# Performance work log

Measured on AMD Instinct MI355X. Metric: run time of the kernel, lower is better.

## Reference

```python
import jax, jax.numpy as jnp
import numpy as np

N_NODES = 40000
N_EDGES = 640000
HIDDEN = 128


def setup_inputs() -> dict:
    key = jax.random.key(0)
    k_h, k_w, k_b, k_src, k_dst = jax.random.split(key, 5)
    h = jax.random.normal(k_h, (N_NODES, HIDDEN), dtype=jnp.float32)
    # nn.Linear(hidden_dim, hidden_dim): weight [out, in], bias [out]
    W = jax.random.normal(k_w, (HIDDEN, HIDDEN), dtype=jnp.float32) * (1.0 / np.sqrt(HIDDEN))
    b = jax.random.normal(k_b, (HIDDEN,), dtype=jnp.float32) * 0.01
    src = jax.random.randint(k_src, (N_EDGES,), 0, N_NODES, dtype=jnp.int32)
    dst = jax.random.randint(k_dst, (N_EDGES,), 0, N_NODES, dtype=jnp.int32)
    return {"h": h, "W": W, "b": b, "src": src, "dst": dst}


def reference(h, W, b, src, dst):
    n = h.shape[0]
    # message: gather source node features; reduce: mailbox sum == segment-sum by dst
    agg = jax.ops.segment_sum(h[src], dst, num_segments=n)  # [N, D]
    updated = agg @ W.T + b  # merge_linner
    # DGL update_all only writes nodes with >=1 incoming edge; others keep old h
    indeg = jax.ops.segment_sum(jnp.ones(src.shape, dtype=h.dtype), dst, num_segments=n)
    return jnp.where((indeg > 0)[:, None], updated, h)
```

## Files before the change

### kernel.cpp

```cpp
#include <hip/hip_runtime.h>
#include <hip/hip_bf16.h>

static constexpr int HIDDEN = 128;

using bf16x8 = __attribute__((ext_vector_type(8))) __bf16;
using f32x4 = __attribute__((ext_vector_type(4))) float;
using ushort8v = __attribute__((ext_vector_type(8))) ushort;

__device__ inline ushort f2bf(float x) {
  __hip_bfloat16 t = __float2bfloat16(x);
  return *reinterpret_cast<ushort*>(&t);
}

__global__ void __launch_bounds__(256) hist_wconv_kernel(
    const int* __restrict__ dst, int* __restrict__ counts, int n_edges,
    int nbh, const float* __restrict__ W, ushort* __restrict__ wbf) {
  if (blockIdx.x < nbh) {
    int i = (blockIdx.x * 256 + threadIdx.x) * 4;
    if (i + 3 < n_edges) {
      int4 d = *reinterpret_cast<const int4*>(dst + i);
      atomicAdd(&counts[d.x], 1);
      atomicAdd(&counts[d.y], 1);
      atomicAdd(&counts[d.z], 1);
      atomicAdd(&counts[d.w], 1);
    } else {
      for (int j = i; j < n_edges; ++j) atomicAdd(&counts[dst[j]], 1);
    }
  } else {
    int i = ((blockIdx.x - nbh) * 256 + threadIdx.x) * 4;
    if (i < HIDDEN * HIDDEN) {
      float4 w = *reinterpret_cast<const float4*>(W + i);
      ushort4 u;
      u.x = f2bf(w.x);
      u.y = f2bf(w.y);
      u.z = f2bf(w.z);
      u.w = f2bf(w.w);
      *reinterpret_cast<ushort4*>(wbf + i) = u;
    }
  }
}

__global__ void __launch_bounds__(256) scanA_kernel(
    const int* __restrict__ counts, int* __restrict__ tilesums, int n) {
  const int t = threadIdx.x;
  const int base = blockIdx.x * 1024 + t * 4;
  int s = 0;
  if (base + 3 < n) {
    int4 v = *reinterpret_cast<const int4*>(counts + base);
    s = v.x + v.y + v.z + v.w;
  } else {
    for (int j = 0; j < 4; ++j)
      if (base + j < n) s += counts[base + j];
  }
  for (int off = 1; off < 64; off <<= 1) s += __shfl_xor(s, off, 64);
  __shared__ int wp[4];
  if ((t & 63) == 0) wp[t >> 6] = s;
  __syncthreads();
  if (t == 0) tilesums[blockIdx.x] = wp[0] + wp[1] + wp[2] + wp[3];
}

__global__ void __launch_bounds__(256) scanC_kernel(
    const int* __restrict__ counts, const int* __restrict__ tilesums,
    int* __restrict__ offsets, int n, int nt) {
  __shared__ int tp[64];
  const int t = threadIdx.x;
  if (t < 64) {
    int v = (t < nt) ? tilesums[t] : 0;
    int orig = v;
    for (int off = 1; off < 64; off <<= 1) {
      int u = __shfl_up(v, off, 64);
      if (t >= off) v += u;
    }
    tp[t] = v - orig;
  }
  __syncthreads();

  const int base = blockIdx.x * 1024 + t * 4;
  int4 v = {0, 0, 0, 0};
  const bool full = (base + 3 < n);
  if (full) {
    v = *reinterpret_cast<const int4*>(counts + base);
  } else {
    if (base + 0 < n) v.x = counts[base + 0];
    if (base + 1 < n) v.y = counts[base + 1];
    if (base + 2 < n) v.z = counts[base + 2];
    if (base + 3 < n) v.w = counts[base + 3];
  }
  const int s = v.x + v.y + v.z + v.w;
  int inc = s;
  for (int off = 1; off < 64; off <<= 1) {
    int u = __shfl_up(inc, off, 64);
    if ((t & 63) >= off) inc += u;
  }
  const int excl = inc - s;
  __shared__ int wp[4];
  if ((t & 63) == 63) wp[t >> 6] = inc;
  __syncthreads();
  int wbase = 0;
  for (int w = 0; w < (t >> 6); ++w) wbase += wp[w];
  int p = tp[blockIdx.x] + wbase + excl;
  if (full) {
    int4 o;
    o.x = p;
    o.y = p + v.x;
    o.z = p + v.x + v.y;
    o.w = p + v.x + v.y + v.z;
    *reinterpret_cast<int4*>(offsets + base) = o;
  } else {
    int run = p;
    if (base + 0 < n) { offsets[base + 0] = run; run += v.x; }
    if (base + 1 < n) { offsets[base + 1] = run; run += v.y; }
    if (base + 2 < n) { offsets[base + 2] = run; run += v.z; }
    if (base + 3 < n) { offsets[base + 3] = run; }
  }
}

__global__ void __launch_bounds__(256) fill_transform_kernel(
    const int* __restrict__ src, const int* __restrict__ dst,
    int* __restrict__ offsets, int* __restrict__ esorted, int n_edges,
    int nbf, const float* __restrict__ h, const ushort* __restrict__ wbf,
    ushort* __restrict__ hW, int n_nodes) {
  constexpr int COLP = 136;
  __shared__ ushort tile[4][16][COLP];

  if (blockIdx.x < nbf) {
    int i = (blockIdx.x * 256 + threadIdx.x) * 4;
    if (i + 3 < n_edges) {
      int4 s = *reinterpret_cast<const int4*>(src + i);
      int4 d = *reinterpret_cast<const int4*>(dst + i);
      int p0 = atomicAdd(&offsets[d.x], 1);
      int p1 = atomicAdd(&offsets[d.y], 1);
      int p2 = atomicAdd(&offsets[d.z], 1);
      int p3 = atomicAdd(&offsets[d.w], 1);
      esorted[p0] = s.x;
      esorted[p1] = s.y;
      esorted[p2] = s.z;
      esorted[p3] = s.w;
    } else {
      for (int j = i; j < n_edges; ++j) {
        int pos = atomicAdd(&offsets[dst[j]], 1);
        esorted[pos] = src[j];
      }
    }
    return;
  }

  const int tb = blockIdx.x - nbf;
  const int wave = threadIdx.x >> 6;
  const int lane = threadIdx.x & 63;
  const int r16 = lane & 15;
  const int kq = lane >> 4;
  const int kbase = kq * 8;
  const int base = tb * 64 + wave * 16;

  int arow = base + r16;
  if (arow >= n_nodes) arow = n_nodes - 1;
  const float* hrow = h + (size_t)arow * HIDDEN;

  bf16x8 a[4];
#pragma unroll
  for (int ks = 0; ks < 4; ++ks) {
    const float4 u = *reinterpret_cast<const float4*>(hrow + ks * 32 + kbase);
    const float4 v =
        *reinterpret_cast<const float4*>(hrow + ks * 32 + kbase + 4);
    bf16x8 t;
    t[0] = (__bf16)u.x;
    t[1] = (__bf16)u.y;
    t[2] = (__bf16)u.z;
    t[3] = (__bf16)u.w;
    t[4] = (__bf16)v.x;
    t[5] = (__bf16)v.y;
    t[6] = (__bf16)v.z;
    t[7] = (__bf16)v.w;
    a[ks] = t;
  }

#pragma unroll
  for (int ct = 0; ct < 8; ++ct) {
    const ushort* wrow = wbf + (size_t)(ct * 16 + r16) * HIDDEN;
    f32x4 acc = {0.f, 0.f, 0.f, 0.f};
#pragma unroll
    for (int ks = 0; ks < 4; ++ks) {
      bf16x8 bfrag = *reinterpret_cast<const bf16x8*>(wrow + ks * 32 + kbase);
      acc = __builtin_amdgcn_mfma_f32_16x16x32_bf16(a[ks], bfrag, acc, 0, 0, 0);
    }
#pragma unroll
    for (int r = 0; r < 4; ++r)
      tile[wave][kq * 4 + r][ct * 16 + r16] = f2bf(acc[r]);
  }
#pragma unroll
  for (int it = 0; it < 4; ++it) {
    const int row = it * 4 + (lane >> 4);
    const int cb = r16 * 8;
    const int nrow = base + row;
    if (nrow < n_nodes) {
      ushort8v v = *reinterpret_cast<const ushort8v*>(&tile[wave][row][cb]);
      *reinterpret_cast<ushort8v*>(hW + (size_t)nrow * HIDDEN + cb) = v;
    }
  }
}

__global__ void __launch_bounds__(256) gather_sum_kernel(
    const ushort* __restrict__ hW, const float* __restrict__ h,
    const float* __restrict__ b, const int* __restrict__ counts,
    const int* __restrict__ ends, const int* __restrict__ esorted,
    float* __restrict__ out, int n_nodes) {
  const int lane = threadIdx.x & 7;
  const int group = threadIdx.x >> 3;
  const int f0 = lane * 16;
  const int node = blockIdx.x * 32 + group;
  if (node >= n_nodes) return;

  const int deg = counts[node];
  f32x4 A = {0.f, 0.f, 0.f, 0.f};
  f32x4 B = {0.f, 0.f, 0.f, 0.f};
  f32x4 C = {0.f, 0.f, 0.f, 0.f};
  f32x4 D = {0.f, 0.f, 0.f, 0.f};
  if (deg == 0) {
    const float* hr = h + (size_t)node * HIDDEN + f0;
    float4 t0 = *reinterpret_cast<const float4*>(hr + 0);
    float4 t1 = *reinterpret_cast<const float4*>(hr + 4);
    float4 t2 = *reinterpret_cast<const float4*>(hr + 8);
    float4 t3 = *reinterpret_cast<const float4*>(hr + 12);
    A = {t0.x, t0.y, t0.z, t0.w};
    B = {t1.x, t1.y, t1.z, t1.w};
    C = {t2.x, t2.y, t2.z, t2.w};
    D = {t3.x, t3.y, t3.z, t3.w};
  } else {
    const int start = ends[node] - deg;
    for (int base = 0; base < deg; base += 8) {
      int sreg = 0;
      if (base + lane < deg)
        sreg = __builtin_nontemporal_load(esorted + start + base + lane);
      const int m = min(8, deg - base);
#pragma unroll 8
      for (int jj = 0; jj < m; ++jj) {
        int s = __shfl(sreg, jj, 8);
        const uint4* rp =
            reinterpret_cast<const uint4*>(hW + (size_t)s * HIDDEN + f0);
        uint4 v0 = rp[0];
        uint4 v1 = rp[1];
        A[0] += __uint_as_float(v0.x << 16);
        A[1] += __uint_as_float(v0.x & 0xffff0000u);
        A[2] += __uint_as_float(v0.y << 16);
        A[3] += __uint_as_float(v0.y & 0xffff0000u);
        B[0] += __uint_as_float(v0.z << 16);
        B[1] += __uint_as_float(v0.z & 0xffff0000u);
        B[2] += __uint_as_float(v0.w << 16);
        B[3] += __uint_as_float(v0.w & 0xffff0000u);
        C[0] += __uint_as_float(v1.x << 16);
        C[1] += __uint_as_float(v1.x & 0xffff0000u);
        C[2] += __uint_as_float(v1.y << 16);
        C[3] += __uint_as_float(v1.y & 0xffff0000u);
        D[0] += __uint_as_float(v1.z << 16);
        D[1] += __uint_as_float(v1.z & 0xffff0000u);
        D[2] += __uint_as_float(v1.w << 16);
        D[3] += __uint_as_float(v1.w & 0xffff0000u);
      }
    }
    const float4 b0 = *reinterpret_cast<const float4*>(b + f0 + 0);
    const float4 b1 = *reinterpret_cast<const float4*>(b + f0 + 4);
    const float4 b2 = *reinterpret_cast<const float4*>(b + f0 + 8);
    const float4 b3 = *reinterpret_cast<const float4*>(b + f0 + 12);
    A[0] += b0.x; A[1] += b0.y; A[2] += b0.z; A[3] += b0.w;
    B[0] += b1.x; B[1] += b1.y; B[2] += b1.z; B[3] += b1.w;
    C[0] += b2.x; C[1] += b2.y; C[2] += b2.z; C[3] += b2.w;
    D[0] += b3.x; D[1] += b3.y; D[2] += b3.z; D[3] += b3.w;
  }
  float* op = out + (size_t)node * HIDDEN + f0;
  __builtin_nontemporal_store(A, reinterpret_cast<f32x4*>(op + 0));
  __builtin_nontemporal_store(B, reinterpret_cast<f32x4*>(op + 4));
  __builtin_nontemporal_store(C, reinterpret_cast<f32x4*>(op + 8));
  __builtin_nontemporal_store(D, reinterpret_cast<f32x4*>(op + 12));
}


__global__ void __launch_bounds__(256) hist_kernel(
    const int* __restrict__ dst, int* __restrict__ counts, int n_edges) {
  int i = blockIdx.x * 256 + threadIdx.x;
  if (i < n_edges) atomicAdd(&counts[dst[i]], 1);
}

__global__ void __launch_bounds__(256) fill1_kernel(
    const int* __restrict__ src, const int* __restrict__ dst,
    int* __restrict__ offsets, int* __restrict__ esorted, int n_edges) {
  int i = blockIdx.x * 256 + threadIdx.x;
  if (i < n_edges) {
    int pos = atomicAdd(&offsets[dst[i]], 1);
    esorted[pos] = src[i];
  }
}

__global__ void __launch_bounds__(1024) scan_kernel(
    const int* __restrict__ counts, int* __restrict__ offsets, int n) {
  __shared__ int part[1024];
  const int t = threadIdx.x;
  const int C = (n + 1023) / 1024;
  const int base = t * C;
  int sum = 0;
  for (int j = 0; j < C; ++j) {
    int idx = base + j;
    if (idx < n) sum += counts[idx];
  }
  part[t] = sum;
  __syncthreads();
  for (int s = 1; s < 1024; s <<= 1) {
    int v = (t >= s) ? part[t - s] : 0;
    __syncthreads();
    part[t] += v;
    __syncthreads();
  }
  int run = part[t] - sum;
  for (int j = 0; j < C; ++j) {
    int idx = base + j;
    if (idx < n) {
      offsets[idx] = run;
      run += counts[idx];
    }
  }
}

__global__ void __launch_bounds__(256, 2) gather_update_kernel(
    const float* __restrict__ h, const float* __restrict__ W,
    const float* __restrict__ b, const int* __restrict__ counts,
    const int* __restrict__ ends, const int* __restrict__ esorted,
    float* __restrict__ out, int n_nodes) {
  __shared__ float Wt[HIDDEN][HIDDEN];
  for (int i = threadIdx.x; i < HIDDEN * HIDDEN / 4; i += 256) {
    int idx = i * 4;
    int j = idx >> 7;
    int k = idx & 127;
    float4 w = *reinterpret_cast<const float4*>(W + j * HIDDEN + k);
    Wt[k + 0][j] = w.x;
    Wt[k + 1][j] = w.y;
    Wt[k + 2][j] = w.z;
    Wt[k + 3][j] = w.w;
  }
  __syncthreads();
  const int lane = threadIdx.x & 31;
  const int group = threadIdx.x >> 5;
  const int j0 = lane * 4;
  const float4 bias = *reinterpret_cast<const float4*>(b + j0);
  const int nb = (n_nodes + 7) >> 3;
  for (int batch = blockIdx.x; batch < nb; batch += gridDim.x) {
    int node = batch * 8 + group;
    if (node >= n_nodes) continue;
    const int deg = counts[node];
    float4 res;
    if (deg == 0) {
      res = reinterpret_cast<const float4*>(h + (size_t)node * HIDDEN)[lane];
    } else {
      const int start = ends[node] - deg;
      float4 acc = {0.f, 0.f, 0.f, 0.f};
      for (int basei = 0; basei < deg; basei += 32) {
        int sreg = 0;
        if (basei + lane < deg) sreg = esorted[start + basei + lane];
        const int m = min(32, deg - basei);
        for (int jj = 0; jj < m; ++jj) {
          int s = __shfl(sreg, jj, 32);
          float4 v =
              reinterpret_cast<const float4*>(h + (size_t)s * HIDDEN)[lane];
          acc.x += v.x;
          acc.y += v.y;
          acc.z += v.z;
          acc.w += v.w;
        }
      }
      const float* av = reinterpret_cast<const float*>(&acc);
      float4 o = bias;
#pragma unroll
      for (int k = 0; k < HIDDEN; ++k) {
        float aval = __shfl(av[k & 3], k >> 2, 32);
        float4 w = *reinterpret_cast<const float4*>(&Wt[k][j0]);
        o.x = fmaf(aval, w.x, o.x);
        o.y = fmaf(aval, w.y, o.y);
        o.z = fmaf(aval, w.z, o.z);
        o.w = fmaf(aval, w.w, o.w);
      }
      res = o;
    }
    reinterpret_cast<float4*>(out + (size_t)node * HIDDEN)[lane] = res;
  }
}


extern "C" void kernel_launch(void* const* d_in, const int* in_sizes, int n_in,
                              void* d_out, int out_size, void* d_ws, size_t ws_size,
                              hipStream_t stream) {
  const float* h = (const float*)d_in[0];
  const float* W = (const float*)d_in[1];
  const float* b = (const float*)d_in[2];
  const int* src = (const int*)d_in[3];
  const int* dst = (const int*)d_in[4];
  float* out = (float*)d_out;
  const int n_nodes = in_sizes[0] / HIDDEN;
  const int n_edges = in_sizes[3];

  const int n_round = (n_nodes + 1023) & ~1023;
  const int nt = n_round / 1024;
  const int eblocks4 = (n_edges + 1023) / 1024;

  int* counts = (int*)d_ws;
  int* offsets = counts + n_round;
  int* tilesums = offsets + n_round;
  int* esorted = tilesums + 64;
  size_t off_bytes = ((size_t)(2 * n_round + 64 + n_edges) * 4 + 15) & ~15ull;
  ushort* hW = (ushort*)((char*)d_ws + off_bytes);
  size_t wbf_off = (off_bytes + (size_t)n_nodes * HIDDEN * 2 + 15) & ~15ull;
  ushort* wbf = (ushort*)((char*)d_ws + wbf_off);
  const size_t need_full = wbf_off + (size_t)HIDDEN * HIDDEN * 2;

  if (ws_size >= need_full && nt <= 64) {
    (void)hipMemsetAsync(counts, 0, (size_t)n_nodes * sizeof(int), stream);
    const int wblocks = (HIDDEN * HIDDEN + 1023) / 1024;
    hist_wconv_kernel<<<eblocks4 + wblocks, 256, 0, stream>>>(
        dst, counts, n_edges, eblocks4, W, wbf);
    scanA_kernel<<<nt, 256, 0, stream>>>(counts, tilesums, n_nodes);
    scanC_kernel<<<nt, 256, 0, stream>>>(counts, tilesums, offsets, n_nodes,
                                         nt);
    const int tblocks = (n_nodes + 63) / 64;
    fill_transform_kernel<<<eblocks4 + tblocks, 256, 0, stream>>>(
        src, dst, offsets, esorted, n_edges, eblocks4, h, wbf, hW, n_nodes);
    const int gblocks = (n_nodes + 31) / 32;
    gather_sum_kernel<<<gblocks, 256, 0, stream>>>(hW, h, b, counts, offsets,
                                                   esorted, out, n_nodes);
  } else {
    (void)hipMemsetAsync(counts, 0, (size_t)n_nodes * sizeof(int), stream);
    const int eblocks = (n_edges + 255) / 256;
    hist_kernel<<<eblocks, 256, 0, stream>>>(dst, counts, n_edges);
    scan_kernel<<<1, 1024, 0, stream>>>(counts, offsets, n_nodes);
    fill1_kernel<<<eblocks, 256, 0, stream>>>(src, dst, offsets, esorted,
                                              n_edges);
    gather_update_kernel<<<512, 256, 0, stream>>>(h, W, b, counts, offsets,
                                                  esorted, out, n_nodes);
  }
}
```

Before: 177.8 us.

## Move node transform into histogram kernel and split out W conversion

The h·W^T MFMA transform now runs as extra blocks of the histogram kernel instead of the fill kernel, and W-to-bf16 conversion moves into its own small kernel launched first. Edge-side blocks change from four edges per thread with int4 loads to one edge per thread. The aim is to overlap the dense transform with the histogram atomics and make the fill kernel lighter. The cost is one more kernel launch and loss of the vectorized edge loads.

```diff
diff --git a/kernel.cpp b/kernel.cpp
--- a/kernel.cpp
+++ b/kernel.cpp
@@ -12,30 +12,84 @@
   return *reinterpret_cast<ushort*>(&t);
 }
 
-__global__ void __launch_bounds__(256) hist_wconv_kernel(
+__global__ void __launch_bounds__(256) wconv_kernel(
+    const float* __restrict__ W, ushort* __restrict__ wbf) {
+  int i = (blockIdx.x * 256 + threadIdx.x) * 4;
+  if (i < HIDDEN * HIDDEN) {
+    float4 w = *reinterpret_cast<const float4*>(W + i);
+    ushort4 u;
+    u.x = f2bf(w.x);
+    u.y = f2bf(w.y);
+    u.z = f2bf(w.z);
+    u.w = f2bf(w.w);
+    *reinterpret_cast<ushort4*>(wbf + i) = u;
+  }
+}
+
+__global__ void __launch_bounds__(256) hist_transform_kernel(
     const int* __restrict__ dst, int* __restrict__ counts, int n_edges,
-    int nbh, const float* __restrict__ W, ushort* __restrict__ wbf) {
+    int nbh, const float* __restrict__ h, const ushort* __restrict__ wbf,
+    ushort* __restrict__ hW, int n_nodes) {
+  constexpr int COLP = 136;
+  __shared__ ushort tile[4][16][COLP];
+
   if (blockIdx.x < nbh) {
-    int i = (blockIdx.x * 256 + threadIdx.x) * 4;
-    if (i + 3 < n_edges) {
-      int4 d = *reinterpret_cast<const int4*>(dst + i);
-      atomicAdd(&counts[d.x], 1);
-      atomicAdd(&counts[d.y], 1);
-      atomicAdd(&counts[d.z], 1);
-      atomicAdd(&counts[d.w], 1);
-    } else {
-      for (int j = i; j < n_edges; ++j) atomicAdd(&counts[dst[j]], 1);
-    }
-  } else {
-    int i = ((blockIdx.x - nbh) * 256 + threadIdx.x) * 4;
-    if (i < HIDDEN * HIDDEN) {
-      float4 w = *reinterpret_cast<const float4*>(W + i);
-      ushort4 u;
-      u.x = f2bf(w.x);
-      u.y = f2bf(w.y);
-      u.z = f2bf(w.z);
-      u.w = f2bf(w.w);
-      *reinterpret_cast<ushort4*>(wbf + i) = u;
+    int i = blockIdx.x * 256 + threadIdx.x;
+    if (i < n_edges) atomicAdd(&counts[dst[i]], 1);
+    return;
+  }
+
+  const int tb = blockIdx.x - nbh;
+  const int wave = threadIdx.x >> 6;
+  const int lane = threadIdx.x & 63;
+  const int r16 = lane & 15;
+  const int kq = lane >> 4;
+  const int kbase = kq * 8;
+  const int base = tb * 64 + wave * 16;
+
+  int arow = base + r16;
+  if (arow >= n_nodes) arow = n_nodes - 1;
+  const float* hrow = h + (size_t)arow * HIDDEN;
+
+  bf16x8 a[4];
+#pragma unroll
+  for (int ks = 0; ks < 4; ++ks) {
+    const float4 u = *reinterpret_cast<const float4*>(hrow + ks * 32 + kbase);
+    const float4 v =
+        *reinterpret_cast<const float4*>(hrow + ks * 32 + kbase + 4);
+    bf16x8 t;
+    t[0] = (__bf16)u.x;
+    t[1] = (__bf16)u.y;
+    t[2] = (__bf16)u.z;
+    t[3] = (__bf16)u.w;
+    t[4] = (__bf16)v.x;
+    t[5] = (__bf16)v.y;
+    t[6] = (__bf16)v.z;
+    t[7] = (__bf16)v.w;
+    a[ks] = t;
+  }
+
+#pragma unroll
+  for (int ct = 0; ct < 8; ++ct) {
+    const ushort* wrow = wbf + (size_t)(ct * 16 + r16) * HIDDEN;
+    f32x4 acc = {0.f, 0.f, 0.f, 0.f};
+#pragma unroll
+    for (int ks = 0; ks < 4; ++ks) {
+      bf16x8 bfrag = *reinterpret_cast<const bf16x8*>(wrow + ks * 32 + kbase);
+      acc = __builtin_amdgcn_mfma_f32_16x16x32_bf16(a[ks], bfrag, acc, 0, 0, 0);
+    }
+#pragma unroll
+    for (int r = 0; r < 4; ++r)
+      tile[wave][kq * 4 + r][ct * 16 + r16] = f2bf(acc[r]);
+  }
+#pragma unroll
+  for (int it = 0; it < 4; ++it) {
+    const int row = it * 4 + (lane >> 4);
+    const int cb = r16 * 8;
+    const int nrow = base + row;
+    if (nrow < n_nodes) {
+      ushort8v v = *reinterpret_cast<const ushort8v*>(&tile[wave][row][cb]);
+      *reinterpret_cast<ushort8v*>(hW + (size_t)nrow * HIDDEN + cb) = v;
     }
   }
 }
@@ -115,88 +169,13 @@
   }
 }
 
-__global__ void __launch_bounds__(256) fill_transform_kernel(
+__global__ void __launch_bounds__(256) fill_kernel(
     const int* __restrict__ src, const int* __restrict__ dst,
-    int* __restrict__ offsets, int* __restrict__ esorted, int n_edges,
-    int nbf, const float* __restrict__ h, const ushort* __restrict__ wbf,
-    ushort* __restrict__ hW, int n_nodes) {
-  constexpr int COLP = 136;
-  __shared__ ushort tile[4][16][COLP];
-
-  if (blockIdx.x < nbf) {
-    int i = (blockIdx.x * 256 + threadIdx.x) * 4;
-    if (i + 3 < n_edges) {
-      int4 s = *reinterpret_cast<const int4*>(src + i);
-      int4 d = *reinterpret_cast<const int4*>(dst + i);
-      int p0 = atomicAdd(&offsets[d.x], 1);
-      int p1 = atomicAdd(&offsets[d.y], 1);
-      int p2 = atomicAdd(&offsets[d.z], 1);
-      int p3 = atomicAdd(&offsets[d.w], 1);
-      esorted[p0] = s.x;
-      esorted[p1] = s.y;
-      esorted[p2] = s.z;
-      esorted[p3] = s.w;
-    } else {
-      for (int j = i; j < n_edges; ++j) {
-        int pos = atomicAdd(&offsets[dst[j]], 1);
-        esorted[pos] = src[j];
-      }
-    }
-    return;
-  }
-
-  const int tb = blockIdx.x - nbf;
-  const int wave = threadIdx.x >> 6;
-  const int lane = threadIdx.x & 63;
-  const int r16 = lane & 15;
-  const int kq = lane >> 4;
-  const int kbase = kq * 8;
-  const int base = tb * 64 + wave * 16;
-
-  int arow = base + r16;
-  if (arow >= n_nodes) arow = n_nodes - 1;
-  const float* hrow = h + (size_t)arow * HIDDEN;
-
-  bf16x8 a[4];
-#pragma unroll
-  for (int ks = 0; ks < 4; ++ks) {
-    const float4 u = *reinterpret_cast<const float4*>(hrow + ks * 32 + kbase);
-    const float4 v =
-        *reinterpret_cast<const float4*>(hrow + ks * 32 + kbase + 4);
-    bf16x8 t;
-    t[0] = (__bf16)u.x;
-    t[1] = (__bf16)u.y;
-    t[2] = (__bf16)u.z;
-    t[3] = (__bf16)u.w;
-    t[4] = (__bf16)v.x;
-    t[5] = (__bf16)v.y;
-    t[6] = (__bf16)v.z;
-    t[7] = (__bf16)v.w;
-    a[ks] = t;
-  }
-
-#pragma unroll
-  for (int ct = 0; ct < 8; ++ct) {
-    const ushort* wrow = wbf + (size_t)(ct * 16 + r16) * HIDDEN;
-    f32x4 acc = {0.f, 0.f, 0.f, 0.f};
-#pragma unroll
-    for (int ks = 0; ks < 4; ++ks) {
-      bf16x8 bfrag = *reinterpret_cast<const bf16x8*>(wrow + ks * 32 + kbase);
-      acc = __builtin_amdgcn_mfma_f32_16x16x32_bf16(a[ks], bfrag, acc, 0, 0, 0);
-    }
-#pragma unroll
-    for (int r = 0; r < 4; ++r)
-      tile[wave][kq * 4 + r][ct * 16 + r16] = f2bf(acc[r]);
-  }
-#pragma unroll
-  for (int it = 0; it < 4; ++it) {
-    const int row = it * 4 + (lane >> 4);
-    const int cb = r16 * 8;
-    const int nrow = base + row;
-    if (nrow < n_nodes) {
-      ushort8v v = *reinterpret_cast<const ushort8v*>(&tile[wave][row][cb]);
-      *reinterpret_cast<ushort8v*>(hW + (size_t)nrow * HIDDEN + cb) = v;
-    }
+    int* __restrict__ offsets, int* __restrict__ esorted, int n_edges) {
+  int i = blockIdx.x * 256 + threadIdx.x;
+  if (i < n_edges) {
+    int pos = atomicAdd(&offsets[dst[i]], 1);
+    esorted[pos] = src[i];
   }
 }
 
@@ -281,16 +260,6 @@
   if (i < n_edges) atomicAdd(&counts[dst[i]], 1);
 }
 
-__global__ void __launch_bounds__(256) fill1_kernel(
-    const int* __restrict__ src, const int* __restrict__ dst,
-    int* __restrict__ offsets, int* __restrict__ esorted, int n_edges) {
-  int i = blockIdx.x * 256 + threadIdx.x;
-  if (i < n_edges) {
-    int pos = atomicAdd(&offsets[dst[i]], 1);
-    esorted[pos] = src[i];
-  }
-}
-
 __global__ void __launch_bounds__(1024) scan_kernel(
     const int* __restrict__ counts, int* __restrict__ offsets, int n) {
   __shared__ int part[1024];
@@ -398,7 +367,7 @@
 
   const int n_round = (n_nodes + 1023) & ~1023;
   const int nt = n_round / 1024;
-  const int eblocks4 = (n_edges + 1023) / 1024;
+  const int eblocks1 = (n_edges + 255) / 256;
 
   int* counts = (int*)d_ws;
   int* offsets = counts + n_round;
@@ -412,24 +381,24 @@
 
   if (ws_size >= need_full && nt <= 64) {
     (void)hipMemsetAsync(counts, 0, (size_t)n_nodes * sizeof(int), stream);
-    const int wblocks = (HIDDEN * HIDDEN + 1023) / 1024;
-    hist_wconv_kernel<<<eblocks4 + wblocks, 256, 0, stream>>>(
-        dst, counts, n_edges, eblocks4, W, wbf);
+    wconv_kernel<<<(HIDDEN * HIDDEN / 4 + 255) / 256, 256, 0, stream>>>(W,
+                                                                        wbf);
+    const int tblocks = (n_nodes + 63) / 64;
+    hist_transform_kernel<<<eblocks1 + tblocks, 256, 0, stream>>>(
+        dst, counts, n_edges, eblocks1, h, wbf, hW, n_nodes);
     scanA_kernel<<<nt, 256, 0, stream>>>(counts, tilesums, n_nodes);
     scanC_kernel<<<nt, 256, 0, stream>>>(counts, tilesums, offsets, n_nodes,
                                          nt);
-    const int tblocks = (n_nodes + 63) / 64;
-    fill_transform_kernel<<<eblocks4 + tblocks, 256, 0, stream>>>(
-        src, dst, offsets, esorted, n_edges, eblocks4, h, wbf, hW, n_nodes);
+    fill_kernel<<<eblocks1, 256, 0, stream>>>(src, dst, offsets, esorted,
+                                              n_edges);
     const int gblocks = (n_nodes + 31) / 32;
     gather_sum_kernel<<<gblocks, 256, 0, stream>>>(hW, h, b, counts, offsets,
                                                    esorted, out, n_nodes);
   } else {
     (void)hipMemsetAsync(counts, 0, (size_t)n_nodes * sizeof(int), stream);
-    const int eblocks = (n_edges + 255) / 256;
-    hist_kernel<<<eblocks, 256, 0, stream>>>(dst, counts, n_edges);
+    hist_kernel<<<eblocks1, 256, 0, stream>>>(dst, counts, n_edges);
     scan_kernel<<<1, 1024, 0, stream>>>(counts, offsets, n_nodes);
-    fill1_kernel<<<eblocks, 256, 0, stream>>>(src, dst, offsets, esorted,
+    fill_kernel<<<eblocks1, 256, 0, stream>>>(src, dst, offsets, esorted,
                                               n_edges);
     gather_update_kernel<<<512, 256, 0, stream>>>(h, W, b, counts, offsets,
                                                   esorted, out, n_nodes);
```

After: 184.3 us. +3.7%, slower.
